# Performance work log

Hardware: AMD Instinct MI355X
Metric: run time of the kernel (lower is better)

## Reference

```python
import jax, jax.numpy as jnp
import numpy as np

B, NPROP, NCLS, NPTS, NBQ, NCK = 32, 256, 19, 4096, 64, 64
C, QH, VQ = 256, 768, 8


def setup_inputs() -> dict:
    key = jax.random.key(0)
    ks = jax.random.split(key, 12)
    s = 0.02
    return dict(
        sem_cls_logits=jax.random.normal(ks[0], (B, NPROP, NCLS), jnp.float32),
        prop_features=jax.random.normal(ks[1], (B, NPROP, C), jnp.float32),
        box_corners=jax.random.normal(ks[2], (B, NPROP, 8, 3), jnp.float32),
        enc_xyz=jax.random.uniform(ks[3], (B, NPTS, 3), jnp.float32),
        enc_features=jax.random.normal(ks[4], (B, NPTS, C), jnp.float32),
        pc_min=jnp.zeros((B, 3), jnp.float32),
        pc_max=jnp.ones((B, 3), jnp.float32),
        box_query=jax.random.normal(ks[5], (B, NBQ, 8, 3), jnp.float32),
        box_qmask=jnp.ones((B, NBQ), jnp.float32),
        click_query=jax.random.uniform(ks[6], (B, NCK, 3), jnp.float32),
        click_qmask=jnp.ones((B, NCK), jnp.float32),
        gauss_B=jax.random.normal(ks[7], (3, C // 2), jnp.float32),
        box_w1=jax.random.normal(ks[8], (C, QH), jnp.float32) * s,
        box_b1=jnp.zeros((QH,), jnp.float32),
        box_w2=jax.random.normal(ks[9], (QH, VQ * QH), jnp.float32) * s,
        box_b2=jnp.zeros((VQ * QH,), jnp.float32),
        click_w1=jax.random.normal(ks[10], (2 * C, QH), jnp.float32) * s,
        click_b1=jnp.zeros((QH,), jnp.float32),
        click_w2=jax.random.normal(ks[11], (QH, VQ * QH), jnp.float32) * s,
        click_b2=jnp.zeros((VQ * QH,), jnp.float32),
    )


def _mlp(x, w1, b1, w2, b2):
    h = jax.nn.relu(jnp.einsum('bqc,ch->bqh', x, w1) + b1)
    return jnp.einsum('bqh,ho->bqo', h, w2) + b2


def _forward(sem_cls_logits, prop_features, box_corners, enc_xyz, enc_features,
             pc_min, pc_max, box_query, box_qmask, click_query, click_qmask,
             gauss_B, box_w1, box_b1, box_w2, box_b2,
             click_w1, click_b1, click_w2, click_b2):
    bsz = sem_cls_logits.shape[0]
    # proposal semantic mask: 0 for background (last class)
    prop_sem_mask = (jnp.argmax(sem_cls_logits, -1) != sem_cls_logits.shape[-1] - 1)
    prop_sem_mask = prop_sem_mask.astype(prop_features.dtype)  # [B, nprop]

    # ---- box branch: axis-aligned 3D IoU from box corners, argmax match, gather ----
    mn_p = box_corners.min(-2)  # [B, nprop, 3]
    mx_p = box_corners.max(-2)
    vol_p = jnp.prod(mx_p - mn_p, -1)  # [B, nprop]
    mn_q = box_query.min(-2)   # [B, nq, 3]
    mx_q = box_query.max(-2)
    vol_q = jnp.prod(mx_q - mn_q, -1)  # [B, nq]
    inter = jnp.prod(
        jnp.clip(jnp.minimum(mx_q[:, :, None], mx_p[:, None]) -
                 jnp.maximum(mn_q[:, :, None], mn_p[:, None]), 0.0, None), -1)  # [B,nq,nprop]
    iou = inter / (vol_q[:, :, None] + vol_p[:, None] - inter + 1e-8)
    iou = iou * prop_sem_mask[:, None, :]
    match_idx = jnp.argmax(iou, -1)  # [B, nq]
    box_feat = jnp.take_along_axis(prop_features, match_idx[..., None], axis=1)  # [B,nq,C]
    box_prompt = _mlp(box_feat, box_w1, box_b1, box_w2, box_b2).reshape(bsz, -1, QH)
    box_mask = jnp.repeat(box_qmask[:, :, None], VQ, axis=2).reshape(bsz, -1)

    # ---- click branch: fourier pos emb + nearest-neighbor gather + MLP ----
    xyz01 = (click_query - pc_min[:, None]) / (pc_max - pc_min)[:, None]
    proj = (xyz01 * (2.0 * jnp.pi)) @ gauss_B  # [B, nclick, C//2]
    pos = jnp.concatenate([jnp.sin(proj), jnp.cos(proj)], -1)  # [B, nclick, C]
    # squared distances (argmin equivalent to cdist argmin)
    d2 = jnp.sum((click_query[:, :, None, :] - enc_xyz[:, None, :, :]) ** 2, -1)  # [B,nclick,npts]
    nn_ids = jnp.argmin(d2, -1)  # [B, nclick]
    k_fea = jnp.take_along_axis(enc_features, nn_ids[..., None], axis=1)  # [B,nclick,C]
    click_in = jnp.concatenate([k_fea, pos], -1)  # [B, nclick, 2C]
    click_prompt = _mlp(click_in, click_w1, click_b1, click_w2, click_b2).reshape(bsz, -1, QH)
    click_mask = jnp.repeat(click_qmask[:, :, None], VQ, axis=2).reshape(bsz, -1)

    prompt_feature = jnp.concatenate([box_prompt, click_prompt], axis=1)  # [B,(nq+nclick)*VQ,QH]
    prompt_mask = jnp.concatenate([box_mask, click_mask], axis=1)
    return prompt_feature, prompt_mask


def reference(sem_cls_logits, prop_features, box_corners, enc_xyz, enc_features,
              pc_min, pc_max, box_query, box_qmask, click_query, click_qmask,
              gauss_B, box_w1, box_b1, box_w2, box_b2,
              click_w1, click_b1, click_w2, click_b2):
    return _forward(sem_cls_logits, prop_features, box_corners, enc_xyz, enc_features,
                    pc_min, pc_max, box_query, box_qmask, click_query, click_qmask,
                    gauss_B, box_w1, box_b1, box_w2, box_b2,
                    click_w1, click_b1, click_w2, click_b2)
```

## Files before the change

### kernel.cpp

```cpp
#include <hip/hip_runtime.h>

#define TWO_PI 6.283185307179586f

typedef _Float16 half8 __attribute__((ext_vector_type(8)));
typedef _Float16 half4 __attribute__((ext_vector_type(4)));
typedef float floatx4 __attribute__((ext_vector_type(4)));

__device__ __forceinline__ void async16(const _Float16* g, _Float16* l) {
    __builtin_amdgcn_global_load_lds(
        (const __attribute__((address_space(1))) void*)g,
        (__attribute__((address_space(3))) void*)l, 16, 0, 0);
}

__device__ __forceinline__ void prep_box_body(
    int b, const float* __restrict__ logits, const float* __restrict__ corners,
    const float* __restrict__ box_query, int* __restrict__ match_idx, float* sm)
{
    float* smn  = sm;
    float* smx  = sm + 768;
    float* svol = sm + 1536;
    float* smsk = sm + 1792;
    int t = threadIdx.x;
    {
        const float* c = corners + ((size_t)b*256 + t) * 24;
        float mn0 = c[0], mn1 = c[1], mn2 = c[2];
        float mx0 = mn0, mx1 = mn1, mx2 = mn2;
#pragma unroll
        for (int k = 1; k < 8; k++) {
            float v0 = c[k*3+0], v1 = c[k*3+1], v2 = c[k*3+2];
            mn0 = fminf(mn0, v0); mx0 = fmaxf(mx0, v0);
            mn1 = fminf(mn1, v1); mx1 = fmaxf(mx1, v1);
            mn2 = fminf(mn2, v2); mx2 = fmaxf(mx2, v2);
        }
        smn[t*3+0] = mn0; smn[t*3+1] = mn1; smn[t*3+2] = mn2;
        smx[t*3+0] = mx0; smx[t*3+1] = mx1; smx[t*3+2] = mx2;
        svol[t] = (mx0-mn0)*(mx1-mn1)*(mx2-mn2);
        const float* lg = logits + ((size_t)b*256 + t) * 19;
        float bv = lg[0]; int bi = 0;
#pragma unroll
        for (int k = 1; k < 19; k++) { float v = lg[k]; if (v > bv) { bv = v; bi = k; } }
        smsk[t] = (bi != 18) ? 1.0f : 0.0f;
    }
    __syncthreads();
    if (t < 64) {
        int gq = b*64 + t;
        const float* cq = box_query + (size_t)gq * 24;
        float mn0 = cq[0], mn1 = cq[1], mn2 = cq[2];
        float mx0 = mn0, mx1 = mn1, mx2 = mn2;
#pragma unroll
        for (int k = 1; k < 8; k++) {
            float v0 = cq[k*3+0], v1 = cq[k*3+1], v2 = cq[k*3+2];
            mn0 = fminf(mn0, v0); mx0 = fmaxf(mx0, v0);
            mn1 = fminf(mn1, v1); mx1 = fmaxf(mx1, v1);
            mn2 = fminf(mn2, v2); mx2 = fmaxf(mx2, v2);
        }
        float volq = (mx0-mn0)*(mx1-mn1)*(mx2-mn2);
        float best = -1.0f; int bi = 0;
        for (int p = 0; p < 256; p++) {
            float e0 = fminf(mx0, smx[p*3+0]) - fmaxf(mn0, smn[p*3+0]); e0 = fmaxf(e0, 0.0f);
            float e1 = fminf(mx1, smx[p*3+1]) - fmaxf(mn1, smn[p*3+1]); e1 = fmaxf(e1, 0.0f);
            float e2 = fminf(mx2, smx[p*3+2]) - fmaxf(mn2, smn[p*3+2]); e2 = fmaxf(e2, 0.0f);
            float inter = (e0*e1)*e2;
            float iou = inter / (volq + svol[p] - inter + 1e-8f) * smsk[p];
            if (iou > best) { best = iou; bi = p; }
        }
        match_idx[gq] = bi;
    }
}

__device__ __forceinline__ void transpose_core(
    const float* __restrict__ src, _Float16* __restrict__ dst,
    int K, int N, _Float16* t, int bx, int by)
{
    int n0 = bx * 64, k0 = by * 64;
    int tid = threadIdx.x;
    int r = tid >> 4;
    int c4 = (tid & 15) * 4;
#pragma unroll
    for (int p = 0; p < 4; p++) {
        int k = r + p*16;
        float4 v = *(const float4*)(src + (size_t)(k0+k)*N + n0 + c4);
        t[(c4+0)*68 + k] = (_Float16)v.x;
        t[(c4+1)*68 + k] = (_Float16)v.y;
        t[(c4+2)*68 + k] = (_Float16)v.z;
        t[(c4+3)*68 + k] = (_Float16)v.w;
    }
    __syncthreads();
    int ck = (tid & 15) * 4;
#pragma unroll
    for (int p = 0; p < 4; p++) {
        int n = r + p*16;
        half4 v = *(const half4*)(t + n*68 + ck);
        *(half4*)(dst + (size_t)(n0+n)*K + k0 + ck) = v;
    }
}

__global__ void prep_fused(
    const float* __restrict__ logits, const float* __restrict__ corners,
    const float* __restrict__ box_query, int* __restrict__ match_idx,
    const float* __restrict__ bw1, const float* __restrict__ cw1,
    _Float16* __restrict__ w1t_box, _Float16* __restrict__ w1t_clk,
    const float* __restrict__ bw2, const float* __restrict__ cw2,
    _Float16* __restrict__ w2t_box, _Float16* __restrict__ w2t_clk)
{
    __shared__ float smem[2176];
    int bid = blockIdx.x;
    if (bid < 2304) {
        _Float16* tb = (_Float16*)smem;
        int x = bid % 96, y = (bid / 96) % 12, z = bid / 1152;
        if (z == 0) transpose_core(bw2, w2t_box, 768, 6144, tb, x, y);
        else        transpose_core(cw2, w2t_clk, 768, 6144, tb, x, y);
    } else if (bid < 2496) {
        _Float16* tb = (_Float16*)smem;
        int r = bid - 2304;
        int x = r % 12, y = (r / 12) % 8, z = r / 96;
        if (z == 0) {
            if (y < 4) transpose_core(bw1, w1t_box, 256, 768, tb, x, y);
        } else {
            transpose_core(cw1, w1t_clk, 512, 768, tb, x, y);
        }
    } else {
        prep_box_body(bid - 2496, logits, corners, box_query, match_idx, smem);
    }
}

__global__ void gather_nn(const float* __restrict__ prop_features,
                          const float* __restrict__ enc_features,
                          const float* __restrict__ enc_xyz,
                          const int* __restrict__ match_idx,
                          const float* __restrict__ cq,
                          const float* __restrict__ pc_min,
                          const float* __restrict__ pc_max,
                          const float* __restrict__ gB,
                          const float* __restrict__ box_qmask,
                          const float* __restrict__ click_qmask,
                          _Float16* __restrict__ box_in,
                          _Float16* __restrict__ click_in,
                          float* __restrict__ out)
{
    __shared__ float rd[4];
    __shared__ int   ri[4];
    __shared__ int   s_nn;
    int row = blockIdx.x;
    int t = threadIdx.x;
    int b = row >> 6;
    int lane = t & 63, wave = t >> 6;

    float cx = cq[row*3+0];
    float cy = cq[row*3+1];
    float cz = cq[row*3+2];
    const float* ex = enc_xyz + (size_t)b * 4096 * 3;
    float best = 3.4e38f; int bidx = 0;
#pragma unroll
    for (int i = 0; i < 16; i++) {
        int p = t + i*256;
        float dx = cx - ex[p*3+0];
        float dy = cy - ex[p*3+1];
        float dz = cz - ex[p*3+2];
        float d = dx*dx + dy*dy;
        d = d + dz*dz;
        if (d < best) { best = d; bidx = p; }
    }
#pragma unroll
    for (int off = 32; off; off >>= 1) {
        float ov = __shfl_down(best, off);
        int   oi = __shfl_down(bidx, off);
        if (ov < best || (ov == best && oi < bidx)) { best = ov; bidx = oi; }
    }
    if (lane == 0) { rd[wave] = best; ri[wave] = bidx; }
    __syncthreads();
    if (t == 0) {
        float bv = rd[0]; int bi = ri[0];
#pragma unroll
        for (int w = 1; w < 4; w++) {
            if (rd[w] < bv || (rd[w] == bv && ri[w] < bi)) { bv = rd[w]; bi = ri[w]; }
        }
        s_nn = bi;
    }
    __syncthreads();
    int nnid = s_nn;

    box_in[(size_t)row*256 + t] =
        (_Float16)prop_features[((size_t)b*256 + match_idx[row])*256 + t];
    click_in[(size_t)row*512 + t] =
        (_Float16)enc_features[((size_t)b*4096 + nnid)*256 + t];
    int j = t & 127;
    float m0 = pc_min[b*3+0], m1 = pc_min[b*3+1], m2 = pc_min[b*3+2];
    float tx = (cx - m0) / (pc_max[b*3+0] - m0) * TWO_PI;
    float ty = (cy - m1) / (pc_max[b*3+1] - m1) * TWO_PI;
    float tz = (cz - m2) / (pc_max[b*3+2] - m2) * TWO_PI;
    float p = tx * gB[j] + ty * gB[128+j] + tz * gB[256+j];
    float v = (t < 128) ? sinf(p) : cosf(p);
    click_in[(size_t)row*512 + 256 + t] = (_Float16)v;
    if (t < 16) {
        int idx = row*16 + t;
        int mb = idx >> 10, i = idx & 1023;
        float mv = (i < 512) ? box_qmask[mb*64 + (i >> 3)]
                             : click_qmask[mb*64 + ((i - 512) >> 3)];
        out[25165824 + idx] = mv;
    }
}

template<int MODE>
__device__ __forceinline__ void gemm_core(
    const _Float16* __restrict__ A, const _Float16* __restrict__ Bt,
    const float* __restrict__ bias, int N, int K,
    _Float16* __restrict__ Hout, float* __restrict__ Fout, long brOff,
    int bm, int bn, _Float16* As, _Float16* Bs)
{
    const int tid = threadIdx.x;
    const int wave = tid >> 6, lane = tid & 63;
    const int waveM = (wave & 1) * 64, waveN = (wave >> 1) * 64;
    const int nrow = lane & 15;
    const int kq   = lane >> 4;

    const int srow = tid >> 3;
    const int jdat = ((tid & 7) ^ (srow & 7)) * 8;

    floatx4 acc[4][4];
#pragma unroll
    for (int i = 0; i < 4; i++)
#pragma unroll
        for (int j = 0; j < 4; j++) { floatx4 z = {0.f,0.f,0.f,0.f}; acc[i][j] = z; }

    const _Float16* Ab[4]; const _Float16* Bb[4];
    _Float16 *lA[4], *lB[4];
#pragma unroll
    for (int q = 0; q < 4; q++) {
        Ab[q] = A  + (size_t)(bm*128 + q*32 + srow) * K + jdat;
        Bb[q] = Bt + (size_t)(bn*128 + q*32 + srow) * K + jdat;
        lA[q] = As + q*2048 + wave*512;
        lB[q] = Bs + q*2048 + wave*512;
    }

    for (int kk = 0; kk < K; kk += 64) {
        __syncthreads();
#pragma unroll
        for (int q = 0; q < 4; q++) async16(Ab[q] + kk, lA[q]);
#pragma unroll
        for (int q = 0; q < 4; q++) async16(Bb[q] + kk, lB[q]);
        __syncthreads();
#pragma unroll
        for (int h = 0; h < 2; h++) {
            const int sw = (((kq + h*4) ^ (nrow & 7)) * 8);
            half8 af[4], bf[4];
#pragma unroll
            for (int i = 0; i < 4; i++)
                af[i] = *(const half8*)(As + (waveM + i*16 + nrow)*64 + sw);
#pragma unroll
            for (int j = 0; j < 4; j++)
                bf[j] = *(const half8*)(Bs + (waveN + j*16 + nrow)*64 + sw);
#pragma unroll
            for (int i = 0; i < 4; i++)
#pragma unroll
                for (int j = 0; j < 4; j++)
                    acc[i][j] = __builtin_amdgcn_mfma_f32_16x16x32_f16(af[i], bf[j], acc[i][j], 0, 0, 0);
        }
    }

#pragma unroll
    for (int i = 0; i < 4; i++) {
#pragma unroll
        for (int j = 0; j < 4; j++) {
            int col = bn*128 + waveN + j*16 + nrow;
            float bv = bias[col];
#pragma unroll
            for (int r = 0; r < 4; r++) {
                int row = bm*128 + waveM + i*16 + kq*4 + r;
                float v = acc[i][j][r] + bv;
                if (MODE == 0) {
                    v = v > 0.f ? v : 0.f;
                    Hout[(size_t)row * N + col] = (_Float16)v;
                } else {
                    size_t off = (size_t)(row >> 6) * 786432 + (size_t)brOff
                               + (size_t)(row & 63) * 6144 + col;
                    Fout[off] = v;
                }
            }
        }
    }
}

__global__ __launch_bounds__(256) void gemm_l1(
    const _Float16* __restrict__ A0, const _Float16* __restrict__ A1,
    const _Float16* __restrict__ B0, const _Float16* __restrict__ B1,
    const float* __restrict__ b0, const float* __restrict__ b1,
    _Float16* __restrict__ H0, _Float16* __restrict__ H1)
{
    __shared__ _Float16 As[8192];
    __shared__ _Float16 Bs[8192];
    if (blockIdx.z == 0)
        gemm_core<0>(A0, B0, b0, 768, 256, H0, nullptr, 0,
                     blockIdx.x, blockIdx.y, As, Bs);
    else
        gemm_core<0>(A1, B1, b1, 768, 512, H1, nullptr, 0,
                     blockIdx.x, blockIdx.y, As, Bs);
}

__global__ __launch_bounds__(256) void gemm_l2(
    const _Float16* __restrict__ A0, const _Float16* __restrict__ A1,
    const _Float16* __restrict__ B0, const _Float16* __restrict__ B1,
    const float* __restrict__ b0, const float* __restrict__ b1,
    float* __restrict__ out)
{
    __shared__ _Float16 As[8192];
    __shared__ _Float16 Bs[8192];
    int lin = blockIdx.x + 16 * blockIdx.y;
    int xcd = lin & 7;
    int per = lin >> 3;
    int bm  = per & 15;
    int bn  = xcd * 6 + (per >> 4);
    if (blockIdx.z == 0)
        gemm_core<1>(A0, B0, b0, 6144, 768, nullptr, out, 0,      bm, bn, As, Bs);
    else
        gemm_core<1>(A1, B1, b1, 6144, 768, nullptr, out, 393216, bm, bn, As, Bs);
}

extern "C" void kernel_launch(void* const* d_in, const int* in_sizes, int n_in,
                              void* d_out, int out_size, void* d_ws, size_t ws_size,
                              hipStream_t stream)
{
    const float* sem   = (const float*)d_in[0];
    const float* propf = (const float*)d_in[1];
    const float* boxc  = (const float*)d_in[2];
    const float* encx  = (const float*)d_in[3];
    const float* encf  = (const float*)d_in[4];
    const float* pcmin = (const float*)d_in[5];
    const float* pcmax = (const float*)d_in[6];
    const float* boxq  = (const float*)d_in[7];
    const float* boxm  = (const float*)d_in[8];
    const float* clkq  = (const float*)d_in[9];
    const float* clkm  = (const float*)d_in[10];
    const float* gB    = (const float*)d_in[11];
    const float* bw1   = (const float*)d_in[12];
    const float* bb1   = (const float*)d_in[13];
    const float* bw2   = (const float*)d_in[14];
    const float* bb2   = (const float*)d_in[15];
    const float* cw1   = (const float*)d_in[16];
    const float* cb1   = (const float*)d_in[17];
    const float* cw2   = (const float*)d_in[18];
    const float* cb2   = (const float*)d_in[19];
    float* out = (float*)d_out;
    char* ws = (char*)d_ws;

    int* midx    = (int*)(ws + 262144);
    _Float16* box_in   = (_Float16*)(ws + 278528);
    _Float16* click_in = (_Float16*)(ws + 1327104);
    _Float16* h_box    = (_Float16*)(ws + 3424256);
    _Float16* h_click  = (_Float16*)(ws + 6569984);
    _Float16* w1t_box  = (_Float16*)(ws + 9715712);
    _Float16* w2t_box  = (_Float16*)(ws + 10108928);
    _Float16* w1t_clk  = (_Float16*)(ws + 19546112);
    _Float16* w2t_clk  = (_Float16*)(ws + 20332544);

    prep_fused<<<2528, 256, 0, stream>>>(sem, boxc, boxq, midx,
                                         bw1, cw1, w1t_box, w1t_clk,
                                         bw2, cw2, w2t_box, w2t_clk);
    gather_nn<<<2048, 256, 0, stream>>>(propf, encf, encx, midx, clkq,
                                        pcmin, pcmax, gB, boxm, clkm,
                                        box_in, click_in, out);
    gemm_l1<<<dim3(16, 6, 2),  256, 0, stream>>>(box_in, click_in, w1t_box, w1t_clk,
                                                 bb1, cb1, h_box, h_click);
    gemm_l2<<<dim3(16, 48, 2), 256, 0, stream>>>(h_box, h_click, w2t_box, w2t_clk,
                                                 bb2, cb2, out);
}
```

Before: 349.2 us.

## Fuse box IoU matching and NN gather into the weight-transpose prep kernel

Merges the prep and gather kernels into one launch. Each of the 2048 query rows now computes its box IoU argmax in parallel (one proposal per thread, then a wave shuffle and block reduction) instead of 64 threads each looping serially over 256 proposals. The row also gathers its nearest-neighbour and matched features in the same block. This removes one kernel launch, the match_idx round trip through global memory, and the serial IoU loop. In exchange, every row recomputes the proposal min/max boxes and logit argmax, which adds redundant global reads of the corners and logits.

```diff
diff --git a/kernel.cpp b/kernel.cpp
--- a/kernel.cpp
+++ b/kernel.cpp
@@ -10,62 +10,6 @@
     __builtin_amdgcn_global_load_lds(
         (const __attribute__((address_space(1))) void*)g,
         (__attribute__((address_space(3))) void*)l, 16, 0, 0);
-}
-
-__device__ __forceinline__ void prep_box_body(
-    int b, const float* __restrict__ logits, const float* __restrict__ corners,
-    const float* __restrict__ box_query, int* __restrict__ match_idx, float* sm)
-{
-    float* smn  = sm;
-    float* smx  = sm + 768;
-    float* svol = sm + 1536;
-    float* smsk = sm + 1792;
-    int t = threadIdx.x;
-    {
-        const float* c = corners + ((size_t)b*256 + t) * 24;
-        float mn0 = c[0], mn1 = c[1], mn2 = c[2];
-        float mx0 = mn0, mx1 = mn1, mx2 = mn2;
-#pragma unroll
-        for (int k = 1; k < 8; k++) {
-            float v0 = c[k*3+0], v1 = c[k*3+1], v2 = c[k*3+2];
-            mn0 = fminf(mn0, v0); mx0 = fmaxf(mx0, v0);
-            mn1 = fminf(mn1, v1); mx1 = fmaxf(mx1, v1);
-            mn2 = fminf(mn2, v2); mx2 = fmaxf(mx2, v2);
-        }
-        smn[t*3+0] = mn0; smn[t*3+1] = mn1; smn[t*3+2] = mn2;
-        smx[t*3+0] = mx0; smx[t*3+1] = mx1; smx[t*3+2] = mx2;
-        svol[t] = (mx0-mn0)*(mx1-mn1)*(mx2-mn2);
-        const float* lg = logits + ((size_t)b*256 + t) * 19;
-        float bv = lg[0]; int bi = 0;
-#pragma unroll
-        for (int k = 1; k < 19; k++) { float v = lg[k]; if (v > bv) { bv = v; bi = k; } }
-        smsk[t] = (bi != 18) ? 1.0f : 0.0f;
-    }
-    __syncthreads();
-    if (t < 64) {
-        int gq = b*64 + t;
-        const float* cq = box_query + (size_t)gq * 24;
-        float mn0 = cq[0], mn1 = cq[1], mn2 = cq[2];
-        float mx0 = mn0, mx1 = mn1, mx2 = mn2;
-#pragma unroll
-        for (int k = 1; k < 8; k++) {
-            float v0 = cq[k*3+0], v1 = cq[k*3+1], v2 = cq[k*3+2];
-            mn0 = fminf(mn0, v0); mx0 = fmaxf(mx0, v0);
-            mn1 = fminf(mn1, v1); mx1 = fmaxf(mx1, v1);
-            mn2 = fminf(mn2, v2); mx2 = fmaxf(mx2, v2);
-        }
-        float volq = (mx0-mn0)*(mx1-mn1)*(mx2-mn2);
-        float best = -1.0f; int bi = 0;
-        for (int p = 0; p < 256; p++) {
-            float e0 = fminf(mx0, smx[p*3+0]) - fmaxf(mn0, smn[p*3+0]); e0 = fmaxf(e0, 0.0f);
-            float e1 = fminf(mx1, smx[p*3+1]) - fmaxf(mn1, smn[p*3+1]); e1 = fmaxf(e1, 0.0f);
-            float e2 = fminf(mx2, smx[p*3+2]) - fmaxf(mn2, smn[p*3+2]); e2 = fmaxf(e2, 0.0f);
-            float inter = (e0*e1)*e2;
-            float iou = inter / (volq + svol[p] - inter + 1e-8f) * smsk[p];
-            if (iou > best) { best = iou; bi = p; }
-        }
-        match_idx[gq] = bi;
-    }
 }
 
 __device__ __forceinline__ void transpose_core(
@@ -95,22 +39,39 @@
     }
 }
 
-__global__ void prep_fused(
+__global__ void mega_prep(
     const float* __restrict__ logits, const float* __restrict__ corners,
-    const float* __restrict__ box_query, int* __restrict__ match_idx,
+    const float* __restrict__ box_query,
     const float* __restrict__ bw1, const float* __restrict__ cw1,
     _Float16* __restrict__ w1t_box, _Float16* __restrict__ w1t_clk,
     const float* __restrict__ bw2, const float* __restrict__ cw2,
-    _Float16* __restrict__ w2t_box, _Float16* __restrict__ w2t_clk)
+    _Float16* __restrict__ w2t_box, _Float16* __restrict__ w2t_clk,
+    const float* __restrict__ prop_features,
+    const float* __restrict__ enc_features,
+    const float* __restrict__ enc_xyz,
+    const float* __restrict__ cq,
+    const float* __restrict__ pc_min,
+    const float* __restrict__ pc_max,
+    const float* __restrict__ gB,
+    const float* __restrict__ box_qmask,
+    const float* __restrict__ click_qmask,
+    _Float16* __restrict__ box_in,
+    _Float16* __restrict__ click_in,
+    float* __restrict__ out)
 {
     __shared__ float smem[2176];
+    __shared__ float nnd[4]; __shared__ int nni[4];
+    __shared__ float bxd[4]; __shared__ int bxi[4];
+    __shared__ int s_nn, s_match;
     int bid = blockIdx.x;
     if (bid < 2304) {
         _Float16* tb = (_Float16*)smem;
         int x = bid % 96, y = (bid / 96) % 12, z = bid / 1152;
         if (z == 0) transpose_core(bw2, w2t_box, 768, 6144, tb, x, y);
         else        transpose_core(cw2, w2t_clk, 768, 6144, tb, x, y);
-    } else if (bid < 2496) {
+        return;
+    }
+    if (bid < 2496) {
         _Float16* tb = (_Float16*)smem;
         int r = bid - 2304;
         int x = r % 12, y = (r / 12) % 8, z = r / 96;
@@ -119,29 +80,10 @@
         } else {
             transpose_core(cw1, w1t_clk, 512, 768, tb, x, y);
         }
-    } else {
-        prep_box_body(bid - 2496, logits, corners, box_query, match_idx, smem);
-    }
-}
-
-__global__ void gather_nn(const float* __restrict__ prop_features,
-                          const float* __restrict__ enc_features,
-                          const float* __restrict__ enc_xyz,
-                          const int* __restrict__ match_idx,
-                          const float* __restrict__ cq,
-                          const float* __restrict__ pc_min,
-                          const float* __restrict__ pc_max,
-                          const float* __restrict__ gB,
-                          const float* __restrict__ box_qmask,
-                          const float* __restrict__ click_qmask,
-                          _Float16* __restrict__ box_in,
-                          _Float16* __restrict__ click_in,
-                          float* __restrict__ out)
-{
-    __shared__ float rd[4];
-    __shared__ int   ri[4];
-    __shared__ int   s_nn;
-    int row = blockIdx.x;
+        return;
+    }
+
+    int row = bid - 2496;
     int t = threadIdx.x;
     int b = row >> 6;
     int lane = t & 63, wave = t >> 6;
@@ -150,7 +92,7 @@
     float cy = cq[row*3+1];
     float cz = cq[row*3+2];
     const float* ex = enc_xyz + (size_t)b * 4096 * 3;
-    float best = 3.4e38f; int bidx = 0;
+    float nbest = 3.4e38f; int nbidx = 0;
 #pragma unroll
     for (int i = 0; i < 16; i++) {
         int p = t + i*256;
@@ -159,29 +101,75 @@
         float dz = cz - ex[p*3+2];
         float d = dx*dx + dy*dy;
         d = d + dz*dz;
-        if (d < best) { best = d; bidx = p; }
+        if (d < nbest) { nbest = d; nbidx = p; }
     }
 #pragma unroll
     for (int off = 32; off; off >>= 1) {
-        float ov = __shfl_down(best, off);
-        int   oi = __shfl_down(bidx, off);
-        if (ov < best || (ov == best && oi < bidx)) { best = ov; bidx = oi; }
-    }
-    if (lane == 0) { rd[wave] = best; ri[wave] = bidx; }
+        float ov = __shfl_down(nbest, off);
+        int   oi = __shfl_down(nbidx, off);
+        if (ov < nbest || (ov == nbest && oi < nbidx)) { nbest = ov; nbidx = oi; }
+    }
+    if (lane == 0) { nnd[wave] = nbest; nni[wave] = nbidx; }
+
+    float iou; int pidx = t;
+    {
+        const float* c = corners + ((size_t)b*256 + t) * 24;
+        float mn0 = c[0], mn1 = c[1], mn2 = c[2];
+        float mx0 = mn0, mx1 = mn1, mx2 = mn2;
+#pragma unroll
+        for (int k = 1; k < 8; k++) {
+            float v0 = c[k*3+0], v1 = c[k*3+1], v2 = c[k*3+2];
+            mn0 = fminf(mn0, v0); mx0 = fmaxf(mx0, v0);
+            mn1 = fminf(mn1, v1); mx1 = fmaxf(mx1, v1);
+            mn2 = fminf(mn2, v2); mx2 = fmaxf(mx2, v2);
+        }
+        float pvol = (mx0-mn0)*(mx1-mn1)*(mx2-mn2);
+        const float* lg = logits + ((size_t)b*256 + t) * 19;
+        float bv = lg[0]; int bi = 0;
+#pragma unroll
+        for (int k = 1; k < 19; k++) { float v = lg[k]; if (v > bv) { bv = v; bi = k; } }
+        float pmsk = (bi != 18) ? 1.0f : 0.0f;
+
+        const float* qc = box_query + (size_t)row * 24;
+        float qn0 = qc[0], qn1 = qc[1], qn2 = qc[2];
+        float qx0 = qn0, qx1 = qn1, qx2 = qn2;
+#pragma unroll
+        for (int k = 1; k < 8; k++) {
+            float v0 = qc[k*3+0], v1 = qc[k*3+1], v2 = qc[k*3+2];
+            qn0 = fminf(qn0, v0); qx0 = fmaxf(qx0, v0);
+            qn1 = fminf(qn1, v1); qx1 = fmaxf(qx1, v1);
+            qn2 = fminf(qn2, v2); qx2 = fmaxf(qx2, v2);
+        }
+        float qvol = (qx0-qn0)*(qx1-qn1)*(qx2-qn2);
+        float e0 = fminf(qx0, mx0) - fmaxf(qn0, mn0); e0 = fmaxf(e0, 0.0f);
+        float e1 = fminf(qx1, mx1) - fmaxf(qn1, mn1); e1 = fmaxf(e1, 0.0f);
+        float e2 = fminf(qx2, mx2) - fmaxf(qn2, mn2); e2 = fmaxf(e2, 0.0f);
+        float inter = (e0*e1)*e2;
+        iou = inter / (qvol + pvol - inter + 1e-8f) * pmsk;
+    }
+#pragma unroll
+    for (int off = 32; off; off >>= 1) {
+        float ov = __shfl_down(iou, off);
+        int   oi = __shfl_down(pidx, off);
+        if (ov > iou || (ov == iou && oi < pidx)) { iou = ov; pidx = oi; }
+    }
+    if (lane == 0) { bxd[wave] = iou; bxi[wave] = pidx; }
     __syncthreads();
     if (t == 0) {
-        float bv = rd[0]; int bi = ri[0];
+        float nv = nnd[0]; int ni = nni[0];
+        float bv = bxd[0]; int bi = bxi[0];
 #pragma unroll
         for (int w = 1; w < 4; w++) {
-            if (rd[w] < bv || (rd[w] == bv && ri[w] < bi)) { bv = rd[w]; bi = ri[w]; }
-        }
-        s_nn = bi;
+            if (nnd[w] < nv || (nnd[w] == nv && nni[w] < ni)) { nv = nnd[w]; ni = nni[w]; }
+            if (bxd[w] > bv || (bxd[w] == bv && bxi[w] < bi)) { bv = bxd[w]; bi = bxi[w]; }
+        }
+        s_nn = ni; s_match = bi;
     }
     __syncthreads();
-    int nnid = s_nn;
+    int nnid = s_nn, match = s_match;
 
     box_in[(size_t)row*256 + t] =
-        (_Float16)prop_features[((size_t)b*256 + match_idx[row])*256 + t];
+        (_Float16)prop_features[((size_t)b*256 + match)*256 + t];
     click_in[(size_t)row*512 + t] =
         (_Float16)enc_features[((size_t)b*4096 + nnid)*256 + t];
     int j = t & 127;
@@ -343,7 +331,6 @@
     float* out = (float*)d_out;
     char* ws = (char*)d_ws;
 
-    int* midx    = (int*)(ws + 262144);
     _Float16* box_in   = (_Float16*)(ws + 278528);
     _Float16* click_in = (_Float16*)(ws + 1327104);
     _Float16* h_box    = (_Float16*)(ws + 3424256);
@@ -353,10 +340,10 @@
     _Float16* w1t_clk  = (_Float16*)(ws + 19546112);
     _Float16* w2t_clk  = (_Float16*)(ws + 20332544);
 
-    prep_fused<<<2528, 256, 0, stream>>>(sem, boxc, boxq, midx,
-                                         bw1, cw1, w1t_box, w1t_clk,
-                                         bw2, cw2, w2t_box, w2t_clk);
-    gather_nn<<<2048, 256, 0, stream>>>(propf, encf, encx, midx, clkq,
+    mega_prep<<<4544, 256, 0, stream>>>(sem, boxc, boxq,
+                                        bw1, cw1, w1t_box, w1t_clk,
+                                        bw2, cw2, w2t_box, w2t_clk,
+                                        propf, encf, encx, clkq,
                                         pcmin, pcmax, gB, boxm, clkm,
                                         box_in, click_in, out);
     gemm_l1<<<dim3(16, 6, 2),  256, 0, stream>>>(box_in, click_in, w1t_box, w1t_clk,
```

Result: faster. 322.5 us (-7.7%).
